# Performance work log

Measured on AMD Instinct MI355X. Metric: run time of the kernel, lower is better.

The kernel has to match this reference:

```python
import jax, jax.numpy as jnp
import numpy as np
from jax import lax

GRID_SIZE = 5
SPLINE_ORDER = 3
GRID_RANGE = (-1.0, 1.0)
# (cin, cout, kernel, stride, pad) per KAN conv layer
CONVS = [(3, 16, 7, 2, 3), (16, 32, 3, 2, 1), (32, 64, 3, 2, 1)]


def make_grid(in_features):
    # uniform extended knot grid: (in_features, grid_size + 2*order + 1)
    h = (GRID_RANGE[1] - GRID_RANGE[0]) / GRID_SIZE
    g = jnp.arange(-SPLINE_ORDER, GRID_SIZE + SPLINE_ORDER + 1, dtype=jnp.float32) * h + GRID_RANGE[0]
    return jnp.broadcast_to(g, (in_features, g.shape[0]))


def b_splines(x, grid):
    # x: (N, in)  ->  (N, in, grid_size + order) via Cox-de Boor recursion
    x = x[..., None]
    bases = ((x >= grid[:, :-1]) & (x < grid[:, 1:])).astype(x.dtype)
    for k in range(1, SPLINE_ORDER + 1):
        left = (x - grid[:, : -(k + 1)]) / (grid[:, k:-1] - grid[:, : -(k + 1)])
        right = (grid[:, k + 1:] - x) / (grid[:, k + 1:] - grid[:, 1:-k])
        bases = left * bases[..., :-1] + right * bases[..., 1:]
    return bases


def kan_linear(x, grid, base_w, spline_w, spline_scaler):
    # base path: silu(x) @ W_base^T ; spline path: B(x) contracted with scaled spline coeffs
    base = jax.nn.silu(x) @ base_w.T
    bsp = b_splines(x, grid)                      # (N, in, K)
    scaled = spline_w * spline_scaler[..., None]  # (out, in, K)
    spline = jnp.einsum('nik,oik->no', bsp, scaled)
    return base + spline


def max_pool_2x2(x):
    return lax.reduce_window(x, -jnp.inf, lax.max, (1, 1, 2, 2), (1, 1, 2, 2), 'VALID')


def setup_inputs() -> dict:
    key = jax.random.key(0)
    ks = jax.random.split(key, 16)
    inp = {'x': jax.random.uniform(ks[0], (8, 3, 224, 224), dtype=jnp.float32)}
    dims = [(16, 147), (32, 144), (64, 288)]
    i = 1
    for li, (out_f, in_f) in enumerate(dims):
        inp[f'bw{li}'] = jax.random.normal(ks[i], (out_f, in_f), jnp.float32) / np.sqrt(in_f); i += 1
        inp[f'sw{li}'] = jax.random.normal(ks[i], (out_f, in_f, GRID_SIZE + SPLINE_ORDER), jnp.float32) * 0.1; i += 1
        inp[f'sc{li}'] = 1.0 + 0.1 * jax.random.normal(ks[i], (out_f, in_f), jnp.float32); i += 1
    inp['bwc'] = jax.random.normal(ks[i], (200, 64), jnp.float32) / 8.0; i += 1
    inp['swc'] = jax.random.normal(ks[i], (200, 64, GRID_SIZE + SPLINE_ORDER), jnp.float32) * 0.1; i += 1
    inp['scc'] = 1.0 + 0.1 * jax.random.normal(ks[i], (200, 64), jnp.float32)
    return inp


def reference(x, bw0, sw0, sc0, bw1, sw1, sc1, bw2, sw2, sc2, bwc, swc, scc):
    params = [(bw0, sw0, sc0), (bw1, sw1, sc1), (bw2, sw2, sc2)]
    h = x
    for i, (cin, cout, k, s, p) in enumerate(CONVS):
        # unfold: (B, cin*k*k, Ho, Wo) with channel-major patch ordering (matches torch unfold)
        patches = lax.conv_general_dilated_patches(
            h, (k, k), (s, s), [(p, p), (p, p)],
            dimension_numbers=('NCHW', 'OIHW', 'NCHW'))
        B, F_, Ho, Wo = patches.shape
        flat = patches.transpose(0, 2, 3, 1).reshape(-1, F_)  # (B*Ho*Wo, cin*k*k)
        y = kan_linear(flat, make_grid(F_), *params[i])
        h = y.reshape(B, Ho, Wo, cout).transpose(0, 3, 1, 2)
        h = jax.nn.relu(h)
        if i < len(CONVS) - 1:
            h = max_pool_2x2(h)
    h = h.mean(axis=(2, 3))  # adaptive avg pool to 1x1 + flatten -> (B, 64)
    return kan_linear(h, make_grid(h.shape[1]), bwc, swc, scc)
```

## Files before the change

### kernel.cpp

```cpp
#include <hip/hip_runtime.h>

#define DEV __device__ __forceinline__

typedef _Float16 f16x8 __attribute__((ext_vector_type(8)));
typedef float f32x4 __attribute__((ext_vector_type(4)));
typedef unsigned int u32x4 __attribute__((ext_vector_type(4)));

DEV f16x8 kan_feats8(float x) {
    const float sil = x / (1.0f + __expf(-x));
    const float k0 = (float)(-3) * 0.4f - 1.0f;
    const float t = (x - k0) * 2.5f;
    const float mf = floorf(t);
    const int m = (int)mf;
    const float u = t - mf, v = 1.0f - u;
    const float u2 = u * u, u3 = u2 * u;
    const float N0 = v * v * v * (1.0f / 6.0f);
    const float N1 = (3.0f * u3 - 6.0f * u2 + 4.0f) * (1.0f / 6.0f);
    const float N2 = (-3.0f * u3 + 3.0f * u2 + 3.0f * u + 1.0f) * (1.0f / 6.0f);
    const float N3 = u3 * (1.0f / 6.0f);
    f16x8 g;
    g[0] = (_Float16)sil;
#pragma unroll
    for (int jj = 0; jj < 6; ++jj) {
        const int j = jj + 2;
        float val = 0.0f;
        val = (m == j + 3) ? N0 : val;
        val = (m == j + 2) ? N1 : val;
        val = (m == j + 1) ? N2 : val;
        val = (m == j)     ? N3 : val;
        g[1 + jj] = (_Float16)val;
    }
    g[7] = (_Float16)0.0f;
    return g;
}

DEV void kan_feats9(float x, float* f) {
    f[0] = x / (1.0f + __expf(-x));
    const float k0 = (float)(-3) * 0.4f - 1.0f;
    const float t = (x - k0) * 2.5f;
    const float mf = floorf(t);
    const int m = (int)mf;
    const float u = t - mf, v = 1.0f - u;
    const float u2 = u * u, u3 = u2 * u;
    const float N0 = v * v * v * (1.0f / 6.0f);
    const float N1 = (3.0f * u3 - 6.0f * u2 + 4.0f) * (1.0f / 6.0f);
    const float N2 = (-3.0f * u3 + 3.0f * u2 + 3.0f * u + 1.0f) * (1.0f / 6.0f);
    const float N3 = u3 * (1.0f / 6.0f);
#pragma unroll
    for (int j = 0; j < 8; ++j) {
        float val = 0.0f;
        val = (m == j + 3) ? N0 : val;
        val = (m == j + 2) ? N1 : val;
        val = (m == j + 1) ? N2 : val;
        val = (m == j)     ? N3 : val;
        f[1 + j] = val;
    }
}

__device__ constexpr int d_l0(int ii) {
    const int i = ii > 146 ? 146 : ii;
    const int ci = i / 49, rem = i % 49, kh = rem / 7, kw = rem % 7;
    return ((((kw & 1) * 3 + ci) * 13 + kh) * 19 + (kw >> 1)) * 16;
}
__device__ constexpr int d_l1(int i) {
    const int ch = i / 9, rem = i % 9, kh = rem / 3, kw = rem % 3;
    return ((((kw & 1) * 16 + ch) * 9 + kh) * 5 + (kw >> 1)) * 16;
}

template <int OUT_F, int IN_F>
DEV void pack_oct8(int g, const float* bw, const float* sw, const float* sc,
                   _Float16* W2) {
    const int o = g % OUT_F, i = g / OUT_F;
    f16x8 v;
    if (i < IN_F) {
        const int wi = o * IN_F + i;
        const float s = sc[wi];
        v[0] = (_Float16)bw[wi];
#pragma unroll
        for (int t = 1; t <= 6; ++t) v[t] = (_Float16)(sw[wi * 8 + t + 1] * s);
        v[7] = (_Float16)0.0f;
    } else {
#pragma unroll
        for (int t = 0; t < 8; ++t) v[t] = (_Float16)0.0f;
    }
    *(f16x8*)(W2 + g * 8) = v;
}

#define PS0 2368
#define PS1 4608
#define PS2 18432
#define PS3 12800
#define PS4 25088
#define PSUM (PS0 + PS1 + PS2 + PS3 + PS4)

__global__ __launch_bounds__(256) void prep_k(
    const float* __restrict__ bw0, const float* __restrict__ sw0, const float* __restrict__ sc0,
    const float* __restrict__ bw1, const float* __restrict__ sw1, const float* __restrict__ sc1,
    const float* __restrict__ bw2, const float* __restrict__ sw2, const float* __restrict__ sc2,
    const float* __restrict__ bwc, const float* __restrict__ swc, const float* __restrict__ scc,
    _Float16* __restrict__ W2_0, _Float16* __restrict__ W2_1, _Float16* __restrict__ W2_2,
    float* __restrict__ wcT, float* __restrict__ h2) {
    const int e = blockIdx.x * 256 + threadIdx.x;
    if (e < PS0) {
        pack_oct8<16, 147>(e, bw0, sw0, sc0, W2_0);
    } else if (e < PS0 + PS1) {
        pack_oct8<32, 144>(e - PS0, bw1, sw1, sc1, W2_1);
    } else if (e < PS0 + PS1 + PS2) {
        pack_oct8<64, 288>(e - PS0 - PS1, bw2, sw2, sc2, W2_2);
    } else if (e < PS0 + PS1 + PS2 + PS3) {
        const int ee = e - PS0 - PS1 - PS2;
        const int o = ee / 64, i = ee - o * 64;
        const float s = scc[ee];
        wcT[(i * 9 + 0) * 200 + o] = bwc[ee];
#pragma unroll
        for (int t = 0; t < 8; ++t)
            wcT[(i * 9 + 1 + t) * 200 + o] = swc[ee * 8 + t] * s;
    } else if (e < PSUM) {
        h2[e - PS0 - PS1 - PS2 - PS3] = 0.0f;
    }
}

__global__ __launch_bounds__(256, 5) void conv0_k(
    const float* __restrict__ x, const _Float16* __restrict__ W2,
    float* __restrict__ p0) {
    __shared__ __align__(16) _Float16 feats[1482 * 8];
    __shared__ float pb[4 * 8 * 16];
    const int tid = threadIdx.x;
    const int vt = blockIdx.x;
    const int b = vt / 196;
    const int r0 = vt - b * 196;
    const int bh = r0 / 7, bw = r0 - (r0 / 7) * 7;
    const int ih0 = bh * 8 - 3, iw0 = bw * 32 - 3;
    for (int t = tid; t < 1482; t += 256) {
        const int iwh = t % 19;
        int r = t / 19;
        const int ihp = r % 13; r /= 13;
        const int ci = r % 3;
        const int par = r / 3;
        const int ih = ih0 + ihp, iw = iw0 + 2 * iwh + par;
        float xv = 0.0f;
        if (ih >= 0 && ih < 224 && iw >= 0 && iw < 224)
            xv = x[((b * 3 + ci) * 224 + ih) * 224 + iw];
        *(f16x8*)(feats + t * 8) = kan_feats8(xv);
    }
    __syncthreads();
    const int lane = tid & 63, mt = tid >> 6;
    const int l15 = lane & 15, q = lane >> 4;
    const bool q1 = q & 1, q2 = q & 2;
    const char* aBase = (const char*)feats + ((2 * mt) * 19 + l15) * 16;
    const f16x8* __restrict__ Wv = (const f16x8*)W2;
    f32x4 acc = {0.f, 0.f, 0.f, 0.f};
#pragma unroll
    for (int s = 0; s < 37; ++s) {
        const int o0 = d_l0(4 * s), o1 = d_l0(4 * s + 1);
        const int o2 = d_l0(4 * s + 2), o3 = d_l0(4 * s + 3);
        const int e01 = q1 ? o1 : o0;
        const int e23 = q1 ? o3 : o2;
        const int aoff = q2 ? e23 : e01;
        const f16x8 a = *(const f16x8*)(aBase + aoff);
        const f16x8 bf = Wv[(s * 4 + q) * 16 + l15];
        acc = __builtin_amdgcn_mfma_f32_16x16x32_f16(a, bf, acc, 0, 0, 0);
    }
    pb[(mt * 8 + 2 * q + 0) * 16 + l15] = fmaxf(fmaxf(acc[0], 0.f), fmaxf(acc[1], 0.f));
    pb[(mt * 8 + 2 * q + 1) * 16 + l15] = fmaxf(fmaxf(acc[2], 0.f), fmaxf(acc[3], 0.f));
    __syncthreads();
    const int pr = tid >> 7, o = (tid >> 3) & 15, wp = tid & 7;
    const float v = fmaxf(pb[((2 * pr) * 8 + wp) * 16 + o],
                          pb[((2 * pr + 1) * 8 + wp) * 16 + o]);
    p0[((b * 16 + o) * 56 + bh * 2 + pr) * 56 + bw * 8 + wp] = v;
}

__global__ __launch_bounds__(256, 5) void conv1_k(
    const float* __restrict__ p0, const _Float16* __restrict__ W2,
    unsigned int* __restrict__ featP1) {
    __shared__ __align__(16) _Float16 feats[1440 * 8];
    __shared__ float abuf[2 * 32 * 16];
    const int tid = threadIdx.x;
    const int vt = blockIdx.x;
    const int b = vt / 49;
    const int r0 = vt - b * 49;
    const int bh = r0 / 7, bw = r0 - (r0 / 7) * 7;
    const int ih0 = bh * 8 - 1, iw0 = bw * 8 - 1;
    for (int t = tid; t < 1296; t += 256) {
        const int iwp = t % 9;
        int r = t / 9;
        const int ihp = r % 9;
        const int ch = r / 9;
        const int ih = ih0 + ihp, iw = iw0 + iwp;
        float xv = 0.0f;
        if (ih >= 0 && ih < 56 && iw >= 0 && iw < 56)
            xv = p0[((b * 16 + ch) * 56 + ih) * 56 + iw];
        const int slot = (((iwp & 1) * 16 + ch) * 9 + ihp) * 5 + (iwp >> 1);
        *(f16x8*)(feats + slot * 8) = kan_feats8(xv);
    }
    __syncthreads();
    const int lane = tid & 63, w = tid >> 6;
    const int kc = w >> 1, ot = w & 1;
    const int l15 = lane & 15, q = lane >> 4;
    const bool q1 = q & 1, q2 = q & 2;
    const int mh = l15 >> 2, mw = l15 & 3;
    const int ocol = ot * 16 + l15;
    const char* aBase = (const char*)feats + ((2 * mh) * 5 + mw) * 16 + kc * 5760;
    const f16x8* __restrict__ Wv = (const f16x8*)W2;
    f32x4 acc = {0.f, 0.f, 0.f, 0.f};
#pragma unroll
    for (int s = 0; s < 18; ++s) {
        const int o0 = d_l1(4 * s), o1 = d_l1(4 * s + 1);
        const int o2 = d_l1(4 * s + 2), o3 = d_l1(4 * s + 3);
        const int e01 = q1 ? o1 : o0;
        const int e23 = q1 ? o3 : o2;
        const int aoff = q2 ? e23 : e01;
        const f16x8 a = *(const f16x8*)(aBase + aoff);
        const f16x8 bf = Wv[(kc * 72 + s * 4 + q) * 32 + ocol];
        acc = __builtin_amdgcn_mfma_f32_16x16x32_f16(a, bf, acc, 0, 0, 0);
    }
#pragma unroll
    for (int reg = 0; reg < 4; ++reg)
        abuf[(kc * 32 + ocol) * 16 + q * 4 + reg] = acc[reg];
    __syncthreads();
    if (tid < 128) {
        const int o = tid >> 2, pp = tid & 3;
        const int hp = pp >> 1, wp = pp & 1;
        float mx = -1e30f;
#pragma unroll
        for (int dh = 0; dh < 2; ++dh)
#pragma unroll
            for (int dw = 0; dw < 2; ++dw) {
                const int m = (2 * hp + dh) * 4 + 2 * wp + dw;
                const float s = abuf[(0 * 32 + o) * 16 + m] + abuf[(1 * 32 + o) * 16 + m];
                mx = fmaxf(mx, fmaxf(s, 0.0f));
            }
        const f16x8 g = kan_feats8(mx);
        const size_t idx = ((b * 32 + o) * 14 + bh * 2 + hp) * 14 + bw * 2 + wp;
        *(u32x4*)(featP1 + idx * 4) = __builtin_bit_cast(u32x4, g);
    }
}

__global__ __launch_bounds__(256, 4) void conv2_k(
    const unsigned int* __restrict__ fm, const _Float16* __restrict__ W2,
    float* __restrict__ h2) {
    __shared__ __align__(16) unsigned int featW[16 * 132];
    const int tid = threadIdx.x;
    const int task = blockIdx.x;
    const int ks = task % 3, rt = task / 3;
    const int lane = tid & 63, ot = tid >> 6;
    const int q = lane >> 4, l15 = lane & 15;
    const int ocol = ot * 16 + l15;
    const u32x4 F0p = __builtin_bit_cast(u32x4, kan_feats8(0.0f));
    const int i_in = tid & 31, rbase = tid >> 5;
    int hi0[2], wi0[2], pixb[2];
    bool rv[2];
#pragma unroll
    for (int t = 0; t < 2; ++t) {
        const int n = rt * 16 + rbase + t * 8;
        const int wo_ = n % 7, ho_ = (n / 7) % 7, b_ = n / 49;
        rv[t] = (n < 392);
        hi0[t] = ho_ * 2 - 1;
        wi0[t] = wo_ * 2 - 1;
        pixb[t] = b_ * 32 * 14 * 14;
    }
    f32x4 acc = {0.f, 0.f, 0.f, 0.f};
    const f16x8* __restrict__ Wv = (const f16x8*)W2;
    for (int c = ks * 3; c < ks * 3 + 3; ++c) {
        const int ii = c * 32 + i_in;
        const int ci = ii / 9, rem = ii - ci * 9;
        const int kh = rem / 3, kw = rem - kh * 3;
#pragma unroll
        for (int t = 0; t < 2; ++t) {
            const int hi = hi0[t] + kh, wi = wi0[t] + kw;
            const bool v = rv[t] && hi >= 0 && hi < 14 && wi >= 0 && wi < 14;
            u32x4 rec = F0p;
            if (v)
                rec = *(const u32x4*)(fm + (size_t)(pixb[t] + (ci * 14 + hi) * 14 + wi) * 4);
            *(u32x4*)(featW + (rbase + t * 8) * 132 + i_in * 4) = rec;
        }
        __syncthreads();
        const char* arow = (const char*)featW + l15 * 528 + q * 16;
#pragma unroll
        for (int s = 0; s < 8; ++s) {
            const f16x8 a = *(const f16x8*)(arow + s * 64);
            const f16x8 bf = Wv[(c * 32 + s * 4 + q) * 64 + ocol];
            acc = __builtin_amdgcn_mfma_f32_16x16x32_f16(a, bf, acc, 0, 0, 0);
        }
        __syncthreads();
    }
#pragma unroll
    for (int reg = 0; reg < 4; ++reg) {
        const int n = rt * 16 + q * 4 + reg;
        if (n < 392) {
            const int wo_ = n % 7, ho_ = (n / 7) % 7, b_ = n / 49;
            atomicAdd(h2 + ((b_ * 64 + ocol) * 7 + ho_) * 7 + wo_, acc[reg]);
        }
    }
}

__global__ __launch_bounds__(256) void head_k(
    const float* __restrict__ h2, const float* __restrict__ wT,
    float* __restrict__ out) {
    __shared__ float feat[64 * 9];
    const int n = blockIdx.x;
    const int tid = threadIdx.x;
    if (tid < 64) {
        const float* p = h2 + (n * 64 + tid) * 49;
        float s = 0.0f;
        for (int j = 0; j < 49; ++j) s += fmaxf(p[j], 0.0f);
        float f9[9];
        kan_feats9(s / 49.0f, f9);
#pragma unroll
        for (int t = 0; t < 9; ++t) feat[tid * 9 + t] = f9[t];
    }
    __syncthreads();
    for (int o = tid; o < 200; o += 256) {
        float sum = 0.0f;
        for (int j = 0; j < 576; ++j) sum += feat[j] * wT[j * 200 + o];
        out[n * 200 + o] = sum;
    }
}

extern "C" void kernel_launch(void* const* d_in, const int* in_sizes, int n_in,
                              void* d_out, int out_size, void* d_ws, size_t ws_size,
                              hipStream_t stream) {
    const float* x   = (const float*)d_in[0];
    const float* bw0 = (const float*)d_in[1];
    const float* sw0 = (const float*)d_in[2];
    const float* sc0 = (const float*)d_in[3];
    const float* bw1 = (const float*)d_in[4];
    const float* sw1 = (const float*)d_in[5];
    const float* sc1 = (const float*)d_in[6];
    const float* bw2 = (const float*)d_in[7];
    const float* sw2 = (const float*)d_in[8];
    const float* sc2 = (const float*)d_in[9];
    const float* bwc = (const float*)d_in[10];
    const float* swc = (const float*)d_in[11];
    const float* scc = (const float*)d_in[12];
    float* out = (float*)d_out;

    char* ws = (char*)d_ws;
    size_t off = 0;
    auto alloc = [&](size_t nbytes) {
        char* p = ws + off;
        off += (nbytes + 255) & ~(size_t)255;
        return p;
    };
    _Float16* W2_0 = (_Float16*)alloc(PS0 * 16);
    _Float16* W2_1 = (_Float16*)alloc(PS1 * 16);
    _Float16* W2_2 = (_Float16*)alloc(PS2 * 16);
    float* wcT = (float*)alloc(576 * 200 * 4);
    float* h2  = (float*)alloc(8 * 64 * 49 * 4);
    float* p0  = (float*)alloc((size_t)8 * 16 * 56 * 56 * 4);
    unsigned int* featP1 = (unsigned int*)alloc((size_t)8 * 32 * 14 * 14 * 16);

    prep_k<<<(PSUM + 255) / 256, 256, 0, stream>>>(
        bw0, sw0, sc0, bw1, sw1, sc1, bw2, sw2, sc2, bwc, swc, scc,
        W2_0, W2_1, W2_2, wcT, h2);
    conv0_k<<<1568, 256, 0, stream>>>(x, W2_0, p0);
    conv1_k<<<392, 256, 0, stream>>>(p0, W2_1, featP1);
    conv2_k<<<75, 256, 0, stream>>>(featP1, W2_2, h2);
    head_k<<<8, 256, 0, stream>>>(h2, wcT, out);
}
```

Baseline: 134.4 us.

## Fuse all stages into one persistent kernel with grid-wide barriers

Replaces the five separate launches (weight prep, conv0, conv1, conv2, head) with a single persistent kernel of 784 blocks separated by atomic-counter grid barriers. Conv0 tiles are looped twice per block, conv2 is split into 225 smaller tasks (one K-chunk each), and the head is spread over 32 blocks with partial sums. This is meant to remove per-launch overhead and tail gaps between small kernels. In exchange it adds barrier spin costs, relies on all 784 blocks being co-resident (deadlock risk if occupancy is insufficient), and needs an extra memset.

```diff
diff --git a/kernel.cpp b/kernel.cpp
--- a/kernel.cpp
+++ b/kernel.cpp
@@ -93,227 +93,257 @@
 #define PS4 25088
 #define PSUM (PS0 + PS1 + PS2 + PS3 + PS4)
 
-__global__ __launch_bounds__(256) void prep_k(
+#define NBLK 784
+
+DEV void gbar(unsigned int* bars, int k) {
+    __syncthreads();
+    if (threadIdx.x == 0) {
+        unsigned int* cnt = bars + k * 64;
+        unsigned int* flg = cnt + 32;
+        __threadfence();
+        atomicAdd(cnt, 1u);
+        if (blockIdx.x == 0) {
+            while (atomicAdd(cnt, 0u) < (unsigned int)NBLK) __builtin_amdgcn_s_sleep(1);
+            __hip_atomic_store(flg, 1u, __ATOMIC_RELEASE, __HIP_MEMORY_SCOPE_AGENT);
+        } else {
+            while (__hip_atomic_load(flg, __ATOMIC_ACQUIRE, __HIP_MEMORY_SCOPE_AGENT) == 0u)
+                __builtin_amdgcn_s_sleep(4);
+        }
+        __threadfence();
+    }
+    __syncthreads();
+}
+
+__global__ __launch_bounds__(256, 4) void fused_k(
+    const float* __restrict__ x,
     const float* __restrict__ bw0, const float* __restrict__ sw0, const float* __restrict__ sc0,
     const float* __restrict__ bw1, const float* __restrict__ sw1, const float* __restrict__ sc1,
     const float* __restrict__ bw2, const float* __restrict__ sw2, const float* __restrict__ sc2,
     const float* __restrict__ bwc, const float* __restrict__ swc, const float* __restrict__ scc,
     _Float16* __restrict__ W2_0, _Float16* __restrict__ W2_1, _Float16* __restrict__ W2_2,
-    float* __restrict__ wcT, float* __restrict__ h2) {
-    const int e = blockIdx.x * 256 + threadIdx.x;
-    if (e < PS0) {
-        pack_oct8<16, 147>(e, bw0, sw0, sc0, W2_0);
-    } else if (e < PS0 + PS1) {
-        pack_oct8<32, 144>(e - PS0, bw1, sw1, sc1, W2_1);
-    } else if (e < PS0 + PS1 + PS2) {
-        pack_oct8<64, 288>(e - PS0 - PS1, bw2, sw2, sc2, W2_2);
-    } else if (e < PS0 + PS1 + PS2 + PS3) {
-        const int ee = e - PS0 - PS1 - PS2;
-        const int o = ee / 64, i = ee - o * 64;
-        const float s = scc[ee];
-        wcT[(i * 9 + 0) * 200 + o] = bwc[ee];
-#pragma unroll
-        for (int t = 0; t < 8; ++t)
-            wcT[(i * 9 + 1 + t) * 200 + o] = swc[ee * 8 + t] * s;
-    } else if (e < PSUM) {
-        h2[e - PS0 - PS1 - PS2 - PS3] = 0.0f;
-    }
-}
-
-__global__ __launch_bounds__(256, 5) void conv0_k(
-    const float* __restrict__ x, const _Float16* __restrict__ W2,
-    float* __restrict__ p0) {
-    __shared__ __align__(16) _Float16 feats[1482 * 8];
-    __shared__ float pb[4 * 8 * 16];
+    float* __restrict__ wcT, float* __restrict__ h2,
+    float* __restrict__ p0, unsigned int* __restrict__ featP1,
+    float* __restrict__ out, unsigned int* __restrict__ bars) {
+    __shared__ __align__(16) char smem[27136];
     const int tid = threadIdx.x;
-    const int vt = blockIdx.x;
-    const int b = vt / 196;
-    const int r0 = vt - b * 196;
-    const int bh = r0 / 7, bw = r0 - (r0 / 7) * 7;
-    const int ih0 = bh * 8 - 3, iw0 = bw * 32 - 3;
-    for (int t = tid; t < 1482; t += 256) {
-        const int iwh = t % 19;
-        int r = t / 19;
-        const int ihp = r % 13; r /= 13;
-        const int ci = r % 3;
-        const int par = r / 3;
-        const int ih = ih0 + ihp, iw = iw0 + 2 * iwh + par;
-        float xv = 0.0f;
-        if (ih >= 0 && ih < 224 && iw >= 0 && iw < 224)
-            xv = x[((b * 3 + ci) * 224 + ih) * 224 + iw];
-        *(f16x8*)(feats + t * 8) = kan_feats8(xv);
-    }
-    __syncthreads();
-    const int lane = tid & 63, mt = tid >> 6;
-    const int l15 = lane & 15, q = lane >> 4;
-    const bool q1 = q & 1, q2 = q & 2;
-    const char* aBase = (const char*)feats + ((2 * mt) * 19 + l15) * 16;
-    const f16x8* __restrict__ Wv = (const f16x8*)W2;
-    f32x4 acc = {0.f, 0.f, 0.f, 0.f};
-#pragma unroll
-    for (int s = 0; s < 37; ++s) {
-        const int o0 = d_l0(4 * s), o1 = d_l0(4 * s + 1);
-        const int o2 = d_l0(4 * s + 2), o3 = d_l0(4 * s + 3);
-        const int e01 = q1 ? o1 : o0;
-        const int e23 = q1 ? o3 : o2;
-        const int aoff = q2 ? e23 : e01;
-        const f16x8 a = *(const f16x8*)(aBase + aoff);
-        const f16x8 bf = Wv[(s * 4 + q) * 16 + l15];
-        acc = __builtin_amdgcn_mfma_f32_16x16x32_f16(a, bf, acc, 0, 0, 0);
-    }
-    pb[(mt * 8 + 2 * q + 0) * 16 + l15] = fmaxf(fmaxf(acc[0], 0.f), fmaxf(acc[1], 0.f));
-    pb[(mt * 8 + 2 * q + 1) * 16 + l15] = fmaxf(fmaxf(acc[2], 0.f), fmaxf(acc[3], 0.f));
-    __syncthreads();
-    const int pr = tid >> 7, o = (tid >> 3) & 15, wp = tid & 7;
-    const float v = fmaxf(pb[((2 * pr) * 8 + wp) * 16 + o],
-                          pb[((2 * pr + 1) * 8 + wp) * 16 + o]);
-    p0[((b * 16 + o) * 56 + bh * 2 + pr) * 56 + bw * 8 + wp] = v;
-}
-
-__global__ __launch_bounds__(256, 5) void conv1_k(
-    const float* __restrict__ p0, const _Float16* __restrict__ W2,
-    unsigned int* __restrict__ featP1) {
-    __shared__ __align__(16) _Float16 feats[1440 * 8];
-    __shared__ float abuf[2 * 32 * 16];
-    const int tid = threadIdx.x;
-    const int vt = blockIdx.x;
-    const int b = vt / 49;
-    const int r0 = vt - b * 49;
-    const int bh = r0 / 7, bw = r0 - (r0 / 7) * 7;
-    const int ih0 = bh * 8 - 1, iw0 = bw * 8 - 1;
-    for (int t = tid; t < 1296; t += 256) {
-        const int iwp = t % 9;
-        int r = t / 9;
-        const int ihp = r % 9;
-        const int ch = r / 9;
-        const int ih = ih0 + ihp, iw = iw0 + iwp;
-        float xv = 0.0f;
-        if (ih >= 0 && ih < 56 && iw >= 0 && iw < 56)
-            xv = p0[((b * 16 + ch) * 56 + ih) * 56 + iw];
-        const int slot = (((iwp & 1) * 16 + ch) * 9 + ihp) * 5 + (iwp >> 1);
-        *(f16x8*)(feats + slot * 8) = kan_feats8(xv);
-    }
-    __syncthreads();
-    const int lane = tid & 63, w = tid >> 6;
-    const int kc = w >> 1, ot = w & 1;
-    const int l15 = lane & 15, q = lane >> 4;
-    const bool q1 = q & 1, q2 = q & 2;
-    const int mh = l15 >> 2, mw = l15 & 3;
-    const int ocol = ot * 16 + l15;
-    const char* aBase = (const char*)feats + ((2 * mh) * 5 + mw) * 16 + kc * 5760;
-    const f16x8* __restrict__ Wv = (const f16x8*)W2;
-    f32x4 acc = {0.f, 0.f, 0.f, 0.f};
-#pragma unroll
-    for (int s = 0; s < 18; ++s) {
-        const int o0 = d_l1(4 * s), o1 = d_l1(4 * s + 1);
-        const int o2 = d_l1(4 * s + 2), o3 = d_l1(4 * s + 3);
-        const int e01 = q1 ? o1 : o0;
-        const int e23 = q1 ? o3 : o2;
-        const int aoff = q2 ? e23 : e01;
-        const f16x8 a = *(const f16x8*)(aBase + aoff);
-        const f16x8 bf = Wv[(kc * 72 + s * 4 + q) * 32 + ocol];
-        acc = __builtin_amdgcn_mfma_f32_16x16x32_f16(a, bf, acc, 0, 0, 0);
-    }
-#pragma unroll
-    for (int reg = 0; reg < 4; ++reg)
-        abuf[(kc * 32 + ocol) * 16 + q * 4 + reg] = acc[reg];
-    __syncthreads();
-    if (tid < 128) {
-        const int o = tid >> 2, pp = tid & 3;
-        const int hp = pp >> 1, wp = pp & 1;
-        float mx = -1e30f;
-#pragma unroll
-        for (int dh = 0; dh < 2; ++dh)
-#pragma unroll
-            for (int dw = 0; dw < 2; ++dw) {
-                const int m = (2 * hp + dh) * 4 + 2 * wp + dw;
-                const float s = abuf[(0 * 32 + o) * 16 + m] + abuf[(1 * 32 + o) * 16 + m];
-                mx = fmaxf(mx, fmaxf(s, 0.0f));
-            }
-        const f16x8 g = kan_feats8(mx);
-        const size_t idx = ((b * 32 + o) * 14 + bh * 2 + hp) * 14 + bw * 2 + wp;
-        *(u32x4*)(featP1 + idx * 4) = __builtin_bit_cast(u32x4, g);
-    }
-}
-
-__global__ __launch_bounds__(256, 4) void conv2_k(
-    const unsigned int* __restrict__ fm, const _Float16* __restrict__ W2,
-    float* __restrict__ h2) {
-    __shared__ __align__(16) unsigned int featW[16 * 132];
-    const int tid = threadIdx.x;
-    const int task = blockIdx.x;
-    const int ks = task % 3, rt = task / 3;
-    const int lane = tid & 63, ot = tid >> 6;
-    const int q = lane >> 4, l15 = lane & 15;
-    const int ocol = ot * 16 + l15;
-    const u32x4 F0p = __builtin_bit_cast(u32x4, kan_feats8(0.0f));
-    const int i_in = tid & 31, rbase = tid >> 5;
-    int hi0[2], wi0[2], pixb[2];
-    bool rv[2];
-#pragma unroll
-    for (int t = 0; t < 2; ++t) {
-        const int n = rt * 16 + rbase + t * 8;
-        const int wo_ = n % 7, ho_ = (n / 7) % 7, b_ = n / 49;
-        rv[t] = (n < 392);
-        hi0[t] = ho_ * 2 - 1;
-        wi0[t] = wo_ * 2 - 1;
-        pixb[t] = b_ * 32 * 14 * 14;
-    }
-    f32x4 acc = {0.f, 0.f, 0.f, 0.f};
-    const f16x8* __restrict__ Wv = (const f16x8*)W2;
-    for (int c = ks * 3; c < ks * 3 + 3; ++c) {
-        const int ii = c * 32 + i_in;
-        const int ci = ii / 9, rem = ii - ci * 9;
-        const int kh = rem / 3, kw = rem - kh * 3;
+    const int bb = blockIdx.x;
+
+    {
+        const int e = bb * 256 + tid;
+        if (e < PS0) {
+            pack_oct8<16, 147>(e, bw0, sw0, sc0, W2_0);
+        } else if (e < PS0 + PS1) {
+            pack_oct8<32, 144>(e - PS0, bw1, sw1, sc1, W2_1);
+        } else if (e < PS0 + PS1 + PS2) {
+            pack_oct8<64, 288>(e - PS0 - PS1, bw2, sw2, sc2, W2_2);
+        } else if (e < PS0 + PS1 + PS2 + PS3) {
+            const int ee = e - PS0 - PS1 - PS2;
+            const int o = ee / 64, i = ee - o * 64;
+            const float s = scc[ee];
+            wcT[(i * 9 + 0) * 200 + o] = bwc[ee];
+#pragma unroll
+            for (int t = 0; t < 8; ++t)
+                wcT[(i * 9 + 1 + t) * 200 + o] = swc[ee * 8 + t] * s;
+        } else if (e < PSUM) {
+            h2[e - PS0 - PS1 - PS2 - PS3] = 0.0f;
+        }
+    }
+    gbar(bars, 0);
+
+    {
+        _Float16* feats = (_Float16*)smem;
+        float* pb = (float*)(smem + 23712);
+        for (int rep = 0; rep < 2; ++rep) {
+            const int vt = bb + rep * NBLK;
+            const int b = vt / 196;
+            const int r0 = vt - b * 196;
+            const int bh = r0 / 7, bw = r0 - (r0 / 7) * 7;
+            const int ih0 = bh * 8 - 3, iw0 = bw * 32 - 3;
+            for (int t = tid; t < 1482; t += 256) {
+                const int iwh = t % 19;
+                int r = t / 19;
+                const int ihp = r % 13; r /= 13;
+                const int ci = r % 3;
+                const int par = r / 3;
+                const int ih = ih0 + ihp, iw = iw0 + 2 * iwh + par;
+                float xv = 0.0f;
+                if (ih >= 0 && ih < 224 && iw >= 0 && iw < 224)
+                    xv = x[((b * 3 + ci) * 224 + ih) * 224 + iw];
+                *(f16x8*)(feats + t * 8) = kan_feats8(xv);
+            }
+            __syncthreads();
+            const int lane = tid & 63, mt = tid >> 6;
+            const int l15 = lane & 15, q = lane >> 4;
+            const bool q1 = q & 1, q2 = q & 2;
+            const char* aBase = (const char*)feats + ((2 * mt) * 19 + l15) * 16;
+            const f16x8* __restrict__ Wv = (const f16x8*)W2_0;
+            f32x4 acc = {0.f, 0.f, 0.f, 0.f};
+#pragma unroll
+            for (int s = 0; s < 37; ++s) {
+                const int o0 = d_l0(4 * s), o1 = d_l0(4 * s + 1);
+                const int o2 = d_l0(4 * s + 2), o3 = d_l0(4 * s + 3);
+                const int e01 = q1 ? o1 : o0;
+                const int e23 = q1 ? o3 : o2;
+                const int aoff = q2 ? e23 : e01;
+                const f16x8 a = *(const f16x8*)(aBase + aoff);
+                const f16x8 bf = Wv[(s * 4 + q) * 16 + l15];
+                acc = __builtin_amdgcn_mfma_f32_16x16x32_f16(a, bf, acc, 0, 0, 0);
+            }
+            pb[(mt * 8 + 2 * q + 0) * 16 + l15] = fmaxf(fmaxf(acc[0], 0.f), fmaxf(acc[1], 0.f));
+            pb[(mt * 8 + 2 * q + 1) * 16 + l15] = fmaxf(fmaxf(acc[2], 0.f), fmaxf(acc[3], 0.f));
+            __syncthreads();
+            const int pr = tid >> 7, o = (tid >> 3) & 15, wp = tid & 7;
+            const float v = fmaxf(pb[((2 * pr) * 8 + wp) * 16 + o],
+                                  pb[((2 * pr + 1) * 8 + wp) * 16 + o]);
+            p0[((b * 16 + o) * 56 + bh * 2 + pr) * 56 + bw * 8 + wp] = v;
+            __syncthreads();
+        }
+    }
+    gbar(bars, 1);
+
+    if (bb < 392) {
+        _Float16* feats = (_Float16*)smem;
+        float* abuf = (float*)(smem + 23040);
+        const int b = bb / 49;
+        const int r0 = bb - b * 49;
+        const int bh = r0 / 7, bw = r0 - (r0 / 7) * 7;
+        const int ih0 = bh * 8 - 1, iw0 = bw * 8 - 1;
+        for (int t = tid; t < 1296; t += 256) {
+            const int iwp = t % 9;
+            int r = t / 9;
+            const int ihp = r % 9;
+            const int ch = r / 9;
+            const int ih = ih0 + ihp, iw = iw0 + iwp;
+            float xv = 0.0f;
+            if (ih >= 0 && ih < 56 && iw >= 0 && iw < 56)
+                xv = p0[((b * 16 + ch) * 56 + ih) * 56 + iw];
+            const int slot = (((iwp & 1) * 16 + ch) * 9 + ihp) * 5 + (iwp >> 1);
+            *(f16x8*)(feats + slot * 8) = kan_feats8(xv);
+        }
+        __syncthreads();
+        const int lane = tid & 63, w = tid >> 6;
+        const int kc = w >> 1, ot = w & 1;
+        const int l15 = lane & 15, q = lane >> 4;
+        const bool q1 = q & 1, q2 = q & 2;
+        const int mh = l15 >> 2, mw = l15 & 3;
+        const int ocol = ot * 16 + l15;
+        const char* aBase = (const char*)feats + ((2 * mh) * 5 + mw) * 16 + kc * 5760;
+        const f16x8* __restrict__ Wv = (const f16x8*)W2_1;
+        f32x4 acc = {0.f, 0.f, 0.f, 0.f};
+#pragma unroll
+        for (int s = 0; s < 18; ++s) {
+            const int o0 = d_l1(4 * s), o1 = d_l1(4 * s + 1);
+            const int o2 = d_l1(4 * s + 2), o3 = d_l1(4 * s + 3);
+            const int e01 = q1 ? o1 : o0;
+            const int e23 = q1 ? o3 : o2;
+            const int aoff = q2 ? e23 : e01;
+            const f16x8 a = *(const f16x8*)(aBase + aoff);
+            const f16x8 bf = Wv[(kc * 72 + s * 4 + q) * 32 + ocol];
+            acc = __builtin_amdgcn_mfma_f32_16x16x32_f16(a, bf, acc, 0, 0, 0);
+        }
+#pragma unroll
+        for (int reg = 0; reg < 4; ++reg)
+            abuf[(kc * 32 + ocol) * 16 + q * 4 + reg] = acc[reg];
+        __syncthreads();
+        if (tid < 128) {
+            const int o = tid >> 2, pp = tid & 3;
+            const int hp = pp >> 1, wp = pp & 1;
+            float mx = -1e30f;
+#pragma unroll
+            for (int dh = 0; dh < 2; ++dh)
+#pragma unroll
+                for (int dw = 0; dw < 2; ++dw) {
+                    const int m = (2 * hp + dh) * 4 + 2 * wp + dw;
+                    const float s = abuf[(0 * 32 + o) * 16 + m] + abuf[(1 * 32 + o) * 16 + m];
+                    mx = fmaxf(mx, fmaxf(s, 0.0f));
+                }
+            const f16x8 g = kan_feats8(mx);
+            const size_t idx = ((b * 32 + o) * 14 + bh * 2 + hp) * 14 + bw * 2 + wp;
+            *(u32x4*)(featP1 + idx * 4) = __builtin_bit_cast(u32x4, g);
+        }
+    }
+    gbar(bars, 2);
+
+    if (bb < 225) {
+        unsigned int* featW = (unsigned int*)smem;
+        const int c = bb % 9, rt = bb / 9;
+        const int lane = tid & 63, ot = tid >> 6;
+        const int q = lane >> 4, l15 = lane & 15;
+        const int ocol = ot * 16 + l15;
+        const u32x4 F0p = __builtin_bit_cast(u32x4, kan_feats8(0.0f));
+        const int i_in = tid & 31, rbase = tid >> 5;
+        int hi0[2], wi0[2], pixb[2];
+        bool rv[2];
 #pragma unroll
         for (int t = 0; t < 2; ++t) {
-            const int hi = hi0[t] + kh, wi = wi0[t] + kw;
-            const bool v = rv[t] && hi >= 0 && hi < 14 && wi >= 0 && wi < 14;
-            u32x4 rec = F0p;
-            if (v)
-                rec = *(const u32x4*)(fm + (size_t)(pixb[t] + (ci * 14 + hi) * 14 + wi) * 4);
-            *(u32x4*)(featW + (rbase + t * 8) * 132 + i_in * 4) = rec;
+            const int n = rt * 16 + rbase + t * 8;
+            const int wo_ = n % 7, ho_ = (n / 7) % 7, b_ = n / 49;
+            rv[t] = (n < 392);
+            hi0[t] = ho_ * 2 - 1;
+            wi0[t] = wo_ * 2 - 1;
+            pixb[t] = b_ * 32 * 14 * 14;
+        }
+        f32x4 acc = {0.f, 0.f, 0.f, 0.f};
+        const f16x8* __restrict__ Wv = (const f16x8*)W2_2;
+        {
+            const int ii = c * 32 + i_in;
+            const int ci = ii / 9, rem = ii - ci * 9;
+            const int kh = rem / 3, kw = rem - kh * 3;
+#pragma unroll
+            for (int t = 0; t < 2; ++t) {
+                const int hi = hi0[t] + kh, wi = wi0[t] + kw;
+                const bool v = rv[t] && hi >= 0 && hi < 14 && wi >= 0 && wi < 14;
+                u32x4 rec = F0p;
+                if (v)
+                    rec = *(const u32x4*)(featP1 + (size_t)(pixb[t] + (ci * 14 + hi) * 14 + wi) * 4);
+                *(u32x4*)(featW + (rbase + t * 8) * 132 + i_in * 4) = rec;
+            }
+            __syncthreads();
+            const char* arow = (const char*)featW + l15 * 528 + q * 16;
+#pragma unroll
+            for (int s = 0; s < 8; ++s) {
+                const f16x8 a = *(const f16x8*)(arow + s * 64);
+                const f16x8 bf = Wv[(c * 32 + s * 4 + q) * 64 + ocol];
+                acc = __builtin_amdgcn_mfma_f32_16x16x32_f16(a, bf, acc, 0, 0, 0);
+            }
+        }
+#pragma unroll
+        for (int reg = 0; reg < 4; ++reg) {
+            const int n = rt * 16 + q * 4 + reg;
+            if (n < 392) {
+                const int wo_ = n % 7, ho_ = (n / 7) % 7, b_ = n / 49;
+                atomicAdd(h2 + ((b_ * 64 + ocol) * 7 + ho_) * 7 + wo_, acc[reg]);
+            }
+        }
+    }
+    gbar(bars, 3);
+
+    if (bb < 32) {
+        float* feat = (float*)smem;
+        float* psum = (float*)(smem + 2304);
+        const int n = bb >> 2, oc = bb & 3;
+        if (tid < 64) {
+            const float* p = h2 + (n * 64 + tid) * 49;
+            float s = 0.0f;
+            for (int j = 0; j < 49; ++j) s += fmaxf(p[j], 0.0f);
+            float f9[9];
+            kan_feats9(s / 49.0f, f9);
+#pragma unroll
+            for (int t = 0; t < 9; ++t) feat[tid * 9 + t] = f9[t];
         }
         __syncthreads();
-        const char* arow = (const char*)featW + l15 * 528 + q * 16;
-#pragma unroll
-        for (int s = 0; s < 8; ++s) {
-            const f16x8 a = *(const f16x8*)(arow + s * 64);
-            const f16x8 bf = Wv[(c * 32 + s * 4 + q) * 64 + ocol];
-            acc = __builtin_amdgcn_mfma_f32_16x16x32_f16(a, bf, acc, 0, 0, 0);
+        const int js = tid >> 6, ol = tid & 63;
+        if (ol < 50) {
+            const int o = oc * 50 + ol;
+            float sum = 0.0f;
+            for (int j = js * 144; j < js * 144 + 144; ++j)
+                sum += feat[j] * wcT[j * 200 + o];
+            psum[js * 64 + ol] = sum;
         }
         __syncthreads();
-    }
-#pragma unroll
-    for (int reg = 0; reg < 4; ++reg) {
-        const int n = rt * 16 + q * 4 + reg;
-        if (n < 392) {
-            const int wo_ = n % 7, ho_ = (n / 7) % 7, b_ = n / 49;
-            atomicAdd(h2 + ((b_ * 64 + ocol) * 7 + ho_) * 7 + wo_, acc[reg]);
-        }
-    }
-}
-
-__global__ __launch_bounds__(256) void head_k(
-    const float* __restrict__ h2, const float* __restrict__ wT,
-    float* __restrict__ out) {
-    __shared__ float feat[64 * 9];
-    const int n = blockIdx.x;
-    const int tid = threadIdx.x;
-    if (tid < 64) {
-        const float* p = h2 + (n * 64 + tid) * 49;
-        float s = 0.0f;
-        for (int j = 0; j < 49; ++j) s += fmaxf(p[j], 0.0f);
-        float f9[9];
-        kan_feats9(s / 49.0f, f9);
-#pragma unroll
-        for (int t = 0; t < 9; ++t) feat[tid * 9 + t] = f9[t];
-    }
-    __syncthreads();
-    for (int o = tid; o < 200; o += 256) {
-        float sum = 0.0f;
-        for (int j = 0; j < 576; ++j) sum += feat[j] * wT[j * 200 + o];
-        out[n * 200 + o] = sum;
+        if (tid < 50)
+            out[n * 200 + oc * 50 + tid] =
+                psum[tid] + psum[64 + tid] + psum[128 + tid] + psum[192 + tid];
     }
 }
 
@@ -349,12 +379,10 @@
     float* h2  = (float*)alloc(8 * 64 * 49 * 4);
     float* p0  = (float*)alloc((size_t)8 * 16 * 56 * 56 * 4);
     unsigned int* featP1 = (unsigned int*)alloc((size_t)8 * 32 * 14 * 14 * 16);
-
-    prep_k<<<(PSUM + 255) / 256, 256, 0, stream>>>(
-        bw0, sw0, sc0, bw1, sw1, sc1, bw2, sw2, sc2, bwc, swc, scc,
-        W2_0, W2_1, W2_2, wcT, h2);
-    conv0_k<<<1568, 256, 0, stream>>>(x, W2_0, p0);
-    conv1_k<<<392, 256, 0, stream>>>(p0, W2_1, featP1);
-    conv2_k<<<75, 256, 0, stream>>>(featP1, W2_2, h2);
-    head_k<<<8, 256, 0, stream>>>(h2, wcT, out);
-}
+    unsigned int* bars = (unsigned int*)alloc(4 * 64 * sizeof(unsigned int));
+
+    hipMemsetAsync(bars, 0, 4 * 64 * sizeof(unsigned int), stream);
+    fused_k<<<NBLK, 256, 0, stream>>>(
+        x, bw0, sw0, sc0, bw1, sw1, sc1, bw2, sw2, sc2, bwc, swc, scc,
+        W2_0, W2_1, W2_2, wcT, h2, p0, featP1, out, bars);
+}
```

After: 533.9 us. 297% more time.
